# Optimization experiments

Measured on AMD Instinct MI355X. Metric: run time of the kernel, lower is better.

Reference implementation:

```python
import jax, jax.numpy as jnp
import numpy as np

B, S, H, E, I = 2, 2048, 1024, 8, 4096
NUM_SELECT = 2


def setup_inputs() -> dict:
    key = jax.random.key(0)
    ks = jax.random.split(key, 6)
    scale = 0.02
    x = jax.random.normal(ks[0], (B, S, H), dtype=jnp.float32)
    Wg = jax.random.normal(ks[1], (H, E), dtype=jnp.float32) * scale
    W1 = jax.random.normal(ks[2], (E, H, I), dtype=jnp.float32) * scale
    b1 = jnp.zeros((E, I), dtype=jnp.float32)
    W2 = jax.random.normal(ks[3], (E, I, H), dtype=jnp.float32) * scale
    b2 = jnp.zeros((E, H), dtype=jnp.float32)
    return {"x": x, "Wg": Wg, "W1": W1, "b1": b1, "W2": W2, "b2": b2}


def reference(x, Wg, W1, b1, W2, b2):
    b, s, h = x.shape
    e = Wg.shape[1]
    xf = x.reshape(-1, h)                       # [T, H], T = b*s
    T = xf.shape[0]

    logits = xf @ Wg                            # [T, E]
    probs = jax.nn.softmax(logits, axis=-1)
    topk_p, topk_i = jax.lax.top_k(probs, NUM_SELECT)   # [T, k]
    topk_p = topk_p / topk_p.sum(axis=-1, keepdims=True)

    # combine weight per (token, expert): w[t, e] = sum_k topk_p[t, k] * 1[topk_i[t, k] == e]
    # top_k indices within a row are distinct, so scatter-add is exact.
    w = jnp.zeros((T, e), dtype=xf.dtype).at[jnp.arange(T)[:, None], topk_i].add(topk_p)

    # Dense per-expert FFN, weighted combine (weight is 0 for unrouted tokens,
    # so math matches the masked gather/scatter loop of the original).
    out = jnp.zeros_like(xf)
    for ei in range(e):  # small fixed loop over experts
        hdn = jax.nn.silu(xf @ W1[ei] + b1[ei])          # [T, I]
        y = hdn @ W2[ei] + b2[ei]                        # [T, H]
        out = out + w[:, ei:ei + 1] * y
    return out.reshape(b, s, h)
```

## Files before the change

kernel.cpp:

```cpp
#include <hip/hip_runtime.h>
#include <cstdint>
#include <cstddef>

using u16 = unsigned short;
typedef __bf16 bf16x8 __attribute__((ext_vector_type(8)));
typedef float f32x4 __attribute__((ext_vector_type(4)));

#define T_TOK 4096
#define HDIM 1024
#define EXP 8
#define IDIM 4096
#define NROWS 8192
#define PAD_ROWS 8448
#define BM 256
#define MAX_TILES 40

__device__ __forceinline__ u16 f2bf(float f) {
  union { float f; uint32_t u; } v; v.f = f;
  uint32_t u = v.u;
  u += 0x7fffu + ((u >> 16) & 1u);
  return (u16)(u >> 16);
}

__device__ __forceinline__ void async_copy16(const u16* g, u16* s) {
  __builtin_amdgcn_global_load_lds((__attribute__((address_space(1))) void*)(void*)g,
                                   (__attribute__((address_space(3))) void*)s, 16, 0, 0);
}

__global__ __launch_bounds__(256) void gate_kernel(const float* __restrict__ x,
                                                   const float* __restrict__ Wg,
                                                   int* __restrict__ sel_e,
                                                   float* __restrict__ sel_w) {
  int lane = threadIdx.x & 63;
  int wave = threadIdx.x >> 6;
  int t = blockIdx.x * 4 + wave;
  const float* xr = x + (size_t)t * HDIM;
  float p[8];
#pragma unroll
  for (int e = 0; e < 8; ++e) p[e] = 0.f;
#pragma unroll
  for (int i = 0; i < 16; ++i) {
    int h = i * 64 + lane;
    float xv = xr[h];
    const float4* w4 = (const float4*)(Wg + h * 8);
    float4 a = w4[0], b = w4[1];
    p[0] += xv * a.x; p[1] += xv * a.y; p[2] += xv * a.z; p[3] += xv * a.w;
    p[4] += xv * b.x; p[5] += xv * b.y; p[6] += xv * b.z; p[7] += xv * b.w;
  }
#pragma unroll
  for (int e = 0; e < 8; ++e) {
#pragma unroll
    for (int off = 32; off > 0; off >>= 1) p[e] += __shfl_xor(p[e], off);
  }
  if (lane == 0) {
    int e0 = 0; float m0 = p[0];
#pragma unroll
    for (int e = 1; e < 8; ++e) { if (p[e] > m0) { m0 = p[e]; e0 = e; } }
    int e1 = -1; float m1 = -3.4e38f;
#pragma unroll
    for (int e = 0; e < 8; ++e) { if (e != e0 && p[e] > m1) { m1 = p[e]; e1 = e; } }
    float r = expf(m1 - m0);
    float w0 = 1.f / (1.f + r);
    float w1 = r / (1.f + r);
    sel_e[2 * t] = e0; sel_e[2 * t + 1] = e1;
    sel_w[2 * t] = w0; sel_w[2 * t + 1] = w1;
  }
}

__global__ void route_kernel(const int* __restrict__ sel_e, const float* __restrict__ sel_w,
                             int* __restrict__ row_token, float* __restrict__ row_weight,
                             int* __restrict__ tile_e, int* __restrict__ tile_m0,
                             int* __restrict__ tile_nrows, int* __restrict__ num_tiles,
                             int* __restrict__ work_ctr) {
  __shared__ int cnt[EXP], off[EXP], cur[EXP];
  int tid = threadIdx.x;
  if (tid < EXP) { cnt[tid] = 0; cur[tid] = 0; }
  if (tid < 2) work_ctr[tid] = 0;
  __syncthreads();
  for (int i = tid; i < NROWS; i += 256) atomicAdd(&cnt[sel_e[i]], 1);
  __syncthreads();
  if (tid == 0) {
    int running = 0, nt = 0;
    for (int e = 0; e < EXP; ++e) {
      off[e] = running;
      int c = cnt[e];
      int ntile = (c + BM - 1) / BM;
      for (int j = 0; j < ntile; ++j) {
        tile_e[nt] = e;
        tile_m0[nt] = running + j * BM;
        tile_nrows[nt] = min(BM, c - j * BM);
        ++nt;
      }
      running += c;
    }
    *num_tiles = nt;
  }
  __syncthreads();
  for (int i = tid; i < NROWS; i += 256) {
    int e = sel_e[i];
    int pos = off[e] + atomicAdd(&cur[e], 1);
    row_token[pos] = i >> 1;
    row_weight[pos] = sel_w[i];
  }
}

__global__ __launch_bounds__(256) void gather_kernel(const float* __restrict__ x,
                                                     const int* __restrict__ row_token,
                                                     u16* __restrict__ xg) {
  int r = blockIdx.x;
  int tok = row_token[r];
  const float4* xs = (const float4*)(x + (size_t)tok * HDIM);
  float4 v = xs[threadIdx.x];
  ushort4 o;
  o.x = f2bf(v.x); o.y = f2bf(v.y); o.z = f2bf(v.z); o.w = f2bf(v.w);
  *(ushort4*)(xg + (size_t)r * HDIM + threadIdx.x * 4) = o;
}

__global__ __launch_bounds__(256) void transpose_convert(const float* __restrict__ src,
                                                         u16* __restrict__ dst, int R, int C) {
  int eb = blockIdx.z;
  const float* s = src + (size_t)eb * R * C;
  u16* d = dst + (size_t)eb * R * C;
  int cb = blockIdx.x * 64, rb = blockIdx.y * 64;
  __shared__ u16 tile[64][65];
  int tid = threadIdx.x;
#pragma unroll
  for (int i = 0; i < 4; ++i) {
    int idx = i * 256 + tid;
    int r = idx >> 4;
    int cq = (idx & 15) * 4;
    float4 v = *(const float4*)(s + (size_t)(rb + r) * C + cb + cq);
    tile[r][cq]     = f2bf(v.x);
    tile[r][cq + 1] = f2bf(v.y);
    tile[r][cq + 2] = f2bf(v.z);
    tile[r][cq + 3] = f2bf(v.w);
  }
  __syncthreads();
#pragma unroll
  for (int i = 0; i < 4; ++i) {
    int idx = i * 256 + tid;
    int c = idx >> 4;
    int rq = (idx & 15) * 4;
    ushort4 o;
    o.x = tile[rq][c]; o.y = tile[rq + 1][c]; o.z = tile[rq + 2][c]; o.w = tile[rq + 3][c];
    *(ushort4*)(d + (size_t)(cb + c) * R + rb + rq) = o;
  }
}

template <int K, int KS, int NB, bool SECOND>
__global__ __launch_bounds__(512, 2) void ffn_gemm8(
    const u16* __restrict__ A, const u16* __restrict__ B,
    const float* __restrict__ bias, u16* __restrict__ hdn_out,
    float* __restrict__ out, const int* __restrict__ row_token,
    const float* __restrict__ row_weight, const int* __restrict__ tile_e,
    const int* __restrict__ tile_m0, const int* __restrict__ tile_nrows,
    const int* __restrict__ num_tiles, int* __restrict__ work_ctr, int N) {
  constexpr int KT = K / KS / 64;
  constexpr int PER_TILE = NB * KS;

  __shared__ u16 sA[2][2 * 128 * 64];
  __shared__ u16 sB[2][128 * 64];
  __shared__ int s_item;

  int tid = threadIdx.x;
  int lane = tid & 63;
  int wave = tid >> 6;
  int wm = wave >> 2, wn = wave & 3;
  int l15 = lane & 15, quad = lane >> 4;
  int r7 = l15 & 7;

  int c0 = tid, c1 = tid + 512;
  int r0s = c0 >> 3, j0 = ((c0 & 7) ^ (r0s & 7)) * 8;
  int r1s = c1 >> 3, j1 = ((c1 & 7) ^ (r1s & 7)) * 8;

  int jxk[2];
#pragma unroll
  for (int ks = 0; ks < 2; ++ks) jxk[ks] = ((ks * 4 + quad) ^ r7) * 8;

  int total = (*num_tiles) * PER_TILE;

  for (;;) {
    if (tid == 0) s_item = atomicAdd(work_ctr, 1);
    __syncthreads();
    int its = s_item;
    if (its >= total) break;

    int tile = its / PER_TILE;
    int rem = its - tile * PER_TILE;
    int nb = rem % NB;
    int ksp = rem / NB;

    int e = tile_e[tile];
    int row0 = tile_m0[tile];
    int nrows = tile_nrows[tile];
    int n0 = nb * 128;
    int korg = ksp * (K / KS);

    const u16* Ab = A + (size_t)row0 * K + korg;
    const u16* Bb = B + (size_t)e * (size_t)N * K + (size_t)n0 * K + korg;

    auto stageA = [&](int db, int sk, int ha) {
      async_copy16(Ab + (size_t)(ha * 128 + r0s) * K + sk * 64 + j0,
                   &sA[db][ha * 8192 + c0 * 8]);
      async_copy16(Ab + (size_t)(ha * 128 + r1s) * K + sk * 64 + j1,
                   &sA[db][ha * 8192 + c1 * 8]);
    };
    auto stageB = [&](int db, int sk) {
      async_copy16(Bb + (size_t)r0s * K + sk * 64 + j0, &sB[db][c0 * 8]);
      async_copy16(Bb + (size_t)r1s * K + sk * 64 + j1, &sB[db][c1 * 8]);
    };

    f32x4 acc[8][2];
#pragma unroll
    for (int am = 0; am < 8; ++am)
#pragma unroll
      for (int an = 0; an < 2; ++an) acc[am][an] = (f32x4){0.f, 0.f, 0.f, 0.f};

    stageA(0, 0, 0); stageA(0, 0, 1);
    stageB(0, 0);
    stageB(1, 1);
    asm volatile("s_waitcnt vmcnt(2)" ::: "memory");
    __builtin_amdgcn_s_barrier();

    for (int kt = 0; kt < KT; ++kt) {
      int cb = kt & 1, pb = cb ^ 1;
      int ka = kt + 1 < KT ? kt + 1 : KT - 1;
      int kb = kt + 2 < KT ? kt + 2 : KT - 1;
      const u16* sAc = sA[cb];
      const u16* sBc = sB[cb];

      bf16x8 bfr[2][2];
#pragma unroll
      for (int ks = 0; ks < 2; ++ks)
#pragma unroll
        for (int an = 0; an < 2; ++an)
          bfr[an][ks] = *(const bf16x8*)(sBc + ((wn * 2 + an) * 16 + l15) * 64 + jxk[ks]);

      {
        bf16x8 af[4][2];
#pragma unroll
        for (int ks = 0; ks < 2; ++ks)
#pragma unroll
          for (int i = 0; i < 4; ++i)
            af[i][ks] = *(const bf16x8*)(sAc + (wm * 128 + i * 16 + l15) * 64 + jxk[ks]);
        stageA(pb, ka, 0);
        stageA(pb, ka, 1);
        __builtin_amdgcn_s_barrier();
        __builtin_amdgcn_s_setprio(1);
#pragma unroll
        for (int i = 0; i < 4; ++i)
#pragma unroll
          for (int an = 0; an < 2; ++an)
#pragma unroll
            for (int ks = 0; ks < 2; ++ks)
              acc[i][an] = __builtin_amdgcn_mfma_f32_16x16x32_bf16(af[i][ks], bfr[an][ks],
                                                                  acc[i][an], 0, 0, 0);
        __builtin_amdgcn_s_setprio(0);
        __builtin_amdgcn_s_barrier();
      }
      {
        bf16x8 af[4][2];
#pragma unroll
        for (int ks = 0; ks < 2; ++ks)
#pragma unroll
          for (int i = 0; i < 4; ++i)
            af[i][ks] = *(const bf16x8*)(sAc + (wm * 128 + (4 + i) * 16 + l15) * 64 + jxk[ks]);
        stageB(cb, kb);
        asm volatile("s_waitcnt vmcnt(2)" ::: "memory");
        __builtin_amdgcn_s_barrier();
        __builtin_amdgcn_s_setprio(1);
#pragma unroll
        for (int i = 0; i < 4; ++i)
#pragma unroll
          for (int an = 0; an < 2; ++an)
#pragma unroll
            for (int ks = 0; ks < 2; ++ks)
              acc[4 + i][an] = __builtin_amdgcn_mfma_f32_16x16x32_bf16(af[i][ks], bfr[an][ks],
                                                                      acc[4 + i][an], 0, 0, 0);
        __builtin_amdgcn_s_setprio(0);
        __builtin_amdgcn_s_barrier();
      }
    }
    asm volatile("s_waitcnt vmcnt(0)" ::: "memory");

    if constexpr (!SECOND) {
#pragma unroll
      for (int an = 0; an < 2; ++an) {
        int col = n0 + (wn * 2 + an) * 16 + l15;
        float bv = bias[e * N + col];
#pragma unroll
        for (int am = 0; am < 8; ++am) {
#pragma unroll
          for (int r = 0; r < 4; ++r) {
            int lr = wm * 128 + am * 16 + quad * 4 + r;
            if (lr < nrows) {
              float vv = acc[am][an][r] + bv;
              vv = vv / (1.f + __expf(-vv));
              hdn_out[(size_t)(row0 + lr) * N + col] = f2bf(vv);
            }
          }
        }
      }
    } else {
      float bv[2];
#pragma unroll
      for (int an = 0; an < 2; ++an)
        bv[an] = (ksp == 0) ? bias[e * N + n0 + (wn * 2 + an) * 16 + l15] : 0.f;
#pragma unroll
      for (int am = 0; am < 8; ++am) {
#pragma unroll
        for (int r = 0; r < 4; ++r) {
          int lr = wm * 128 + am * 16 + quad * 4 + r;
          if (lr < nrows) {
            int grow = row0 + lr;
            int tok = row_token[grow];
            float w = row_weight[grow];
            float* orow = out + (size_t)tok * N;
#pragma unroll
            for (int an = 0; an < 2; ++an) {
              int col = n0 + (wn * 2 + an) * 16 + l15;
              atomicAdd(orow + col, (acc[am][an][r] + bv[an]) * w);
            }
          }
        }
      }
    }
  }
}

extern "C" void kernel_launch(void* const* d_in, const int* in_sizes, int n_in,
                              void* d_out, int out_size, void* d_ws, size_t ws_size,
                              hipStream_t stream) {
  const float* x  = (const float*)d_in[0];
  const float* Wg = (const float*)d_in[1];
  const float* W1 = (const float*)d_in[2];
  const float* b1 = (const float*)d_in[3];
  const float* W2 = (const float*)d_in[4];
  const float* b2 = (const float*)d_in[5];
  float* out = (float*)d_out;

  char* ws = (char*)d_ws;
  size_t off = 0;
  auto alloc = [&](size_t bytes) {
    void* p = ws + off;
    off += (bytes + 255) & ~(size_t)255;
    return p;
  };
  u16* W1T = (u16*)alloc((size_t)EXP * IDIM * HDIM * 2);
  u16* W2T = (u16*)alloc((size_t)EXP * IDIM * HDIM * 2);
  u16* xg  = (u16*)alloc((size_t)PAD_ROWS * HDIM * 2);
  u16* hdn = (u16*)alloc((size_t)PAD_ROWS * IDIM * 2);
  int*   sel_e      = (int*)alloc(NROWS * 4);
  float* sel_w      = (float*)alloc(NROWS * 4);
  int*   row_token  = (int*)alloc(NROWS * 4);
  float* row_weight = (float*)alloc(NROWS * 4);
  int* tile_e     = (int*)alloc(MAX_TILES * 4);
  int* tile_m0    = (int*)alloc(MAX_TILES * 4);
  int* tile_nrows = (int*)alloc(MAX_TILES * 4);
  int* num_tiles  = (int*)alloc(4);
  int* work_ctr   = (int*)alloc(2 * 4);

  hipMemsetAsync(d_out, 0, (size_t)out_size * sizeof(float), stream);
  transpose_convert<<<dim3(IDIM / 64, HDIM / 64, EXP), 256, 0, stream>>>(W1, W1T, HDIM, IDIM);
  transpose_convert<<<dim3(HDIM / 64, IDIM / 64, EXP), 256, 0, stream>>>(W2, W2T, IDIM, HDIM);
  gate_kernel<<<T_TOK / 4, 256, 0, stream>>>(x, Wg, sel_e, sel_w);
  route_kernel<<<1, 256, 0, stream>>>(sel_e, sel_w, row_token, row_weight,
                                      tile_e, tile_m0, tile_nrows, num_tiles, work_ctr);
  gather_kernel<<<NROWS, 256, 0, stream>>>(x, row_token, xg);
  ffn_gemm8<HDIM, 1, 32, false><<<256, 512, 0, stream>>>(
      xg, W1T, b1, hdn, nullptr, nullptr, nullptr,
      tile_e, tile_m0, tile_nrows, num_tiles, work_ctr + 0, IDIM);
  ffn_gemm8<IDIM, 2, 8, true><<<256, 512, 0, stream>>>(
      hdn, W2T, b2, nullptr, out, row_token, row_weight,
      tile_e, tile_m0, tile_nrows, num_tiles, work_ctr + 1, HDIM);
}
```

Measured before the change: 674.4 us.

## Schedule grouped GEMM work per expert with XCD-affine per-expert work counters

Replaces the single global work counter with eight per-expert counters. Each block starts on the expert matching its XCD index (blockIdx & 7) and moves to the next expert once that one's queue is empty. Within an expert, work items are reordered so the tile index varies fastest, meaning consecutive items share the same weight column block. The aim is to keep each expert's weights resident in one XCD's L2 and to improve weight reuse across tiles. In exchange, blocks may take items from several expert queues near the end, and load balancing is coarser when experts have uneven token counts.

Measured after the change: 682.5 us. About the same (+1.2%).

```diff
diff --git a/kernel.cpp b/kernel.cpp
--- a/kernel.cpp
+++ b/kernel.cpp
@@ -69,13 +69,13 @@
 
 __global__ void route_kernel(const int* __restrict__ sel_e, const float* __restrict__ sel_w,
                              int* __restrict__ row_token, float* __restrict__ row_weight,
-                             int* __restrict__ tile_e, int* __restrict__ tile_m0,
-                             int* __restrict__ tile_nrows, int* __restrict__ num_tiles,
+                             int* __restrict__ tile_m0, int* __restrict__ tile_nrows,
+                             int* __restrict__ tile_start, int* __restrict__ tile_cnt,
                              int* __restrict__ work_ctr) {
   __shared__ int cnt[EXP], off[EXP], cur[EXP];
   int tid = threadIdx.x;
   if (tid < EXP) { cnt[tid] = 0; cur[tid] = 0; }
-  if (tid < 2) work_ctr[tid] = 0;
+  if (tid < 16) work_ctr[tid] = 0;
   __syncthreads();
   for (int i = tid; i < NROWS; i += 256) atomicAdd(&cnt[sel_e[i]], 1);
   __syncthreads();
@@ -85,15 +85,15 @@
       off[e] = running;
       int c = cnt[e];
       int ntile = (c + BM - 1) / BM;
+      tile_start[e] = nt;
+      tile_cnt[e] = ntile;
       for (int j = 0; j < ntile; ++j) {
-        tile_e[nt] = e;
         tile_m0[nt] = running + j * BM;
         tile_nrows[nt] = min(BM, c - j * BM);
         ++nt;
       }
       running += c;
     }
-    *num_tiles = nt;
   }
   __syncthreads();
   for (int i = tid; i < NROWS; i += 256) {
@@ -152,11 +152,10 @@
     const u16* __restrict__ A, const u16* __restrict__ B,
     const float* __restrict__ bias, u16* __restrict__ hdn_out,
     float* __restrict__ out, const int* __restrict__ row_token,
-    const float* __restrict__ row_weight, const int* __restrict__ tile_e,
-    const int* __restrict__ tile_m0, const int* __restrict__ tile_nrows,
-    const int* __restrict__ num_tiles, int* __restrict__ work_ctr, int N) {
+    const float* __restrict__ row_weight, const int* __restrict__ tile_m0,
+    const int* __restrict__ tile_nrows, const int* __restrict__ tile_start,
+    const int* __restrict__ tile_cnt, int* __restrict__ ctr, int N) {
   constexpr int KT = K / KS / 64;
-  constexpr int PER_TILE = NB * KS;
 
   __shared__ u16 sA[2][2 * 128 * 64];
   __shared__ u16 sB[2][128 * 64];
@@ -168,6 +167,7 @@
   int wm = wave >> 2, wn = wave & 3;
   int l15 = lane & 15, quad = lane >> 4;
   int r7 = l15 & 7;
+  int xcd = blockIdx.x & 7;
 
   int c0 = tid, c1 = tid + 512;
   int r0s = c0 >> 3, j0 = ((c0 & 7) ^ (r0s & 7)) * 8;
@@ -177,149 +177,155 @@
 #pragma unroll
   for (int ks = 0; ks < 2; ++ks) jxk[ks] = ((ks * 4 + quad) ^ r7) * 8;
 
-  int total = (*num_tiles) * PER_TILE;
-
-  for (;;) {
-    if (tid == 0) s_item = atomicAdd(work_ctr, 1);
-    __syncthreads();
-    int its = s_item;
-    if (its >= total) break;
-
-    int tile = its / PER_TILE;
-    int rem = its - tile * PER_TILE;
-    int nb = rem % NB;
-    int ksp = rem / NB;
-
-    int e = tile_e[tile];
-    int row0 = tile_m0[tile];
-    int nrows = tile_nrows[tile];
-    int n0 = nb * 128;
-    int korg = ksp * (K / KS);
-
-    const u16* Ab = A + (size_t)row0 * K + korg;
-    const u16* Bb = B + (size_t)e * (size_t)N * K + (size_t)n0 * K + korg;
-
-    auto stageA = [&](int db, int sk, int ha) {
-      async_copy16(Ab + (size_t)(ha * 128 + r0s) * K + sk * 64 + j0,
-                   &sA[db][ha * 8192 + c0 * 8]);
-      async_copy16(Ab + (size_t)(ha * 128 + r1s) * K + sk * 64 + j1,
-                   &sA[db][ha * 8192 + c1 * 8]);
-    };
-    auto stageB = [&](int db, int sk) {
-      async_copy16(Bb + (size_t)r0s * K + sk * 64 + j0, &sB[db][c0 * 8]);
-      async_copy16(Bb + (size_t)r1s * K + sk * 64 + j1, &sB[db][c1 * 8]);
-    };
-
-    f32x4 acc[8][2];
-#pragma unroll
-    for (int am = 0; am < 8; ++am)
-#pragma unroll
-      for (int an = 0; an < 2; ++an) acc[am][an] = (f32x4){0.f, 0.f, 0.f, 0.f};
-
-    stageA(0, 0, 0); stageA(0, 0, 1);
-    stageB(0, 0);
-    stageB(1, 1);
-    asm volatile("s_waitcnt vmcnt(2)" ::: "memory");
-    __builtin_amdgcn_s_barrier();
-
-    for (int kt = 0; kt < KT; ++kt) {
-      int cb = kt & 1, pb = cb ^ 1;
-      int ka = kt + 1 < KT ? kt + 1 : KT - 1;
-      int kb = kt + 2 < KT ? kt + 2 : KT - 1;
-      const u16* sAc = sA[cb];
-      const u16* sBc = sB[cb];
-
-      bf16x8 bfr[2][2];
-#pragma unroll
-      for (int ks = 0; ks < 2; ++ks)
+  for (int pass = 0; pass < 8; ++pass) {
+    int ex = (xcd + pass) & 7;
+    int nt_e = tile_cnt[ex];
+    if (nt_e == 0) continue;
+    int items = nt_e * NB * KS;
+    int ts = tile_start[ex];
+
+    for (;;) {
+      if (tid == 0) s_item = atomicAdd(&ctr[ex], 1);
+      __syncthreads();
+      int its = s_item;
+      if (its >= items) break;
+
+      int per = NB * nt_e;
+      int ksp = its / per;
+      int rem = its - ksp * per;
+      int nb = rem / nt_e;
+      int tile = ts + (rem - nb * nt_e);
+
+      int row0 = tile_m0[tile];
+      int nrows = tile_nrows[tile];
+      int n0 = nb * 128;
+      int korg = ksp * (K / KS);
+
+      const u16* Ab = A + (size_t)row0 * K + korg;
+      const u16* Bb = B + (size_t)ex * (size_t)N * K + (size_t)n0 * K + korg;
+
+      auto stageA = [&](int db, int sk, int ha) {
+        async_copy16(Ab + (size_t)(ha * 128 + r0s) * K + sk * 64 + j0,
+                     &sA[db][ha * 8192 + c0 * 8]);
+        async_copy16(Ab + (size_t)(ha * 128 + r1s) * K + sk * 64 + j1,
+                     &sA[db][ha * 8192 + c1 * 8]);
+      };
+      auto stageB = [&](int db, int sk) {
+        async_copy16(Bb + (size_t)r0s * K + sk * 64 + j0, &sB[db][c0 * 8]);
+        async_copy16(Bb + (size_t)r1s * K + sk * 64 + j1, &sB[db][c1 * 8]);
+      };
+
+      f32x4 acc[8][2];
+#pragma unroll
+      for (int am = 0; am < 8; ++am)
+#pragma unroll
+        for (int an = 0; an < 2; ++an) acc[am][an] = (f32x4){0.f, 0.f, 0.f, 0.f};
+
+      stageA(0, 0, 0); stageA(0, 0, 1);
+      stageB(0, 0);
+      stageB(1, 1);
+      asm volatile("s_waitcnt vmcnt(2)" ::: "memory");
+      __builtin_amdgcn_s_barrier();
+
+      for (int kt = 0; kt < KT; ++kt) {
+        int cb = kt & 1, pb = cb ^ 1;
+        int ka = kt + 1 < KT ? kt + 1 : KT - 1;
+        int kb = kt + 2 < KT ? kt + 2 : KT - 1;
+        const u16* sAc = sA[cb];
+        const u16* sBc = sB[cb];
+
+        bf16x8 bfr[2][2];
+#pragma unroll
+        for (int ks = 0; ks < 2; ++ks)
+#pragma unroll
+          for (int an = 0; an < 2; ++an)
+            bfr[an][ks] = *(const bf16x8*)(sBc + ((wn * 2 + an) * 16 + l15) * 64 + jxk[ks]);
+
+        {
+          bf16x8 af[4][2];
+#pragma unroll
+          for (int ks = 0; ks < 2; ++ks)
+#pragma unroll
+            for (int i = 0; i < 4; ++i)
+              af[i][ks] = *(const bf16x8*)(sAc + (wm * 128 + i * 16 + l15) * 64 + jxk[ks]);
+          stageA(pb, ka, 0);
+          stageA(pb, ka, 1);
+          __builtin_amdgcn_s_barrier();
+          __builtin_amdgcn_s_setprio(1);
+#pragma unroll
+          for (int i = 0; i < 4; ++i)
+#pragma unroll
+            for (int an = 0; an < 2; ++an)
+#pragma unroll
+              for (int ks = 0; ks < 2; ++ks)
+                acc[i][an] = __builtin_amdgcn_mfma_f32_16x16x32_bf16(af[i][ks], bfr[an][ks],
+                                                                    acc[i][an], 0, 0, 0);
+          __builtin_amdgcn_s_setprio(0);
+          __builtin_amdgcn_s_barrier();
+        }
+        {
+          bf16x8 af[4][2];
+#pragma unroll
+          for (int ks = 0; ks < 2; ++ks)
+#pragma unroll
+            for (int i = 0; i < 4; ++i)
+              af[i][ks] = *(const bf16x8*)(sAc + (wm * 128 + (4 + i) * 16 + l15) * 64 + jxk[ks]);
+          stageB(cb, kb);
+          asm volatile("s_waitcnt vmcnt(2)" ::: "memory");
+          __builtin_amdgcn_s_barrier();
+          __builtin_amdgcn_s_setprio(1);
+#pragma unroll
+          for (int i = 0; i < 4; ++i)
+#pragma unroll
+            for (int an = 0; an < 2; ++an)
+#pragma unroll
+              for (int ks = 0; ks < 2; ++ks)
+                acc[4 + i][an] = __builtin_amdgcn_mfma_f32_16x16x32_bf16(af[i][ks], bfr[an][ks],
+                                                                        acc[4 + i][an], 0, 0, 0);
+          __builtin_amdgcn_s_setprio(0);
+          __builtin_amdgcn_s_barrier();
+        }
+      }
+      asm volatile("s_waitcnt vmcnt(0)" ::: "memory");
+
+      if constexpr (!SECOND) {
+#pragma unroll
+        for (int an = 0; an < 2; ++an) {
+          int col = n0 + (wn * 2 + an) * 16 + l15;
+          float bv = bias[ex * N + col];
+#pragma unroll
+          for (int am = 0; am < 8; ++am) {
+#pragma unroll
+            for (int r = 0; r < 4; ++r) {
+              int lr = wm * 128 + am * 16 + quad * 4 + r;
+              if (lr < nrows) {
+                float vv = acc[am][an][r] + bv;
+                vv = vv / (1.f + __expf(-vv));
+                hdn_out[(size_t)(row0 + lr) * N + col] = f2bf(vv);
+              }
+            }
+          }
+        }
+      } else {
+        float bv[2];
 #pragma unroll
         for (int an = 0; an < 2; ++an)
-          bfr[an][ks] = *(const bf16x8*)(sBc + ((wn * 2 + an) * 16 + l15) * 64 + jxk[ks]);
-
-      {
-        bf16x8 af[4][2];
-#pragma unroll
-        for (int ks = 0; ks < 2; ++ks)
-#pragma unroll
-          for (int i = 0; i < 4; ++i)
-            af[i][ks] = *(const bf16x8*)(sAc + (wm * 128 + i * 16 + l15) * 64 + jxk[ks]);
-        stageA(pb, ka, 0);
-        stageA(pb, ka, 1);
-        __builtin_amdgcn_s_barrier();
-        __builtin_amdgcn_s_setprio(1);
-#pragma unroll
-        for (int i = 0; i < 4; ++i)
-#pragma unroll
-          for (int an = 0; an < 2; ++an)
-#pragma unroll
-            for (int ks = 0; ks < 2; ++ks)
-              acc[i][an] = __builtin_amdgcn_mfma_f32_16x16x32_bf16(af[i][ks], bfr[an][ks],
-                                                                  acc[i][an], 0, 0, 0);
-        __builtin_amdgcn_s_setprio(0);
-        __builtin_amdgcn_s_barrier();
-      }
-      {
-        bf16x8 af[4][2];
-#pragma unroll
-        for (int ks = 0; ks < 2; ++ks)
-#pragma unroll
-          for (int i = 0; i < 4; ++i)
-            af[i][ks] = *(const bf16x8*)(sAc + (wm * 128 + (4 + i) * 16 + l15) * 64 + jxk[ks]);
-        stageB(cb, kb);
-        asm volatile("s_waitcnt vmcnt(2)" ::: "memory");
-        __builtin_amdgcn_s_barrier();
-        __builtin_amdgcn_s_setprio(1);
-#pragma unroll
-        for (int i = 0; i < 4; ++i)
-#pragma unroll
-          for (int an = 0; an < 2; ++an)
-#pragma unroll
-            for (int ks = 0; ks < 2; ++ks)
-              acc[4 + i][an] = __builtin_amdgcn_mfma_f32_16x16x32_bf16(af[i][ks], bfr[an][ks],
-                                                                      acc[4 + i][an], 0, 0, 0);
-        __builtin_amdgcn_s_setprio(0);
-        __builtin_amdgcn_s_barrier();
-      }
-    }
-    asm volatile("s_waitcnt vmcnt(0)" ::: "memory");
-
-    if constexpr (!SECOND) {
-#pragma unroll
-      for (int an = 0; an < 2; ++an) {
-        int col = n0 + (wn * 2 + an) * 16 + l15;
-        float bv = bias[e * N + col];
+          bv[an] = (ksp == 0) ? bias[ex * N + n0 + (wn * 2 + an) * 16 + l15] : 0.f;
 #pragma unroll
         for (int am = 0; am < 8; ++am) {
 #pragma unroll
           for (int r = 0; r < 4; ++r) {
             int lr = wm * 128 + am * 16 + quad * 4 + r;
             if (lr < nrows) {
-              float vv = acc[am][an][r] + bv;
-              vv = vv / (1.f + __expf(-vv));
-              hdn_out[(size_t)(row0 + lr) * N + col] = f2bf(vv);
-            }
-          }
-        }
-      }
-    } else {
-      float bv[2];
-#pragma unroll
-      for (int an = 0; an < 2; ++an)
-        bv[an] = (ksp == 0) ? bias[e * N + n0 + (wn * 2 + an) * 16 + l15] : 0.f;
-#pragma unroll
-      for (int am = 0; am < 8; ++am) {
-#pragma unroll
-        for (int r = 0; r < 4; ++r) {
-          int lr = wm * 128 + am * 16 + quad * 4 + r;
-          if (lr < nrows) {
-            int grow = row0 + lr;
-            int tok = row_token[grow];
-            float w = row_weight[grow];
-            float* orow = out + (size_t)tok * N;
-#pragma unroll
-            for (int an = 0; an < 2; ++an) {
-              int col = n0 + (wn * 2 + an) * 16 + l15;
-              atomicAdd(orow + col, (acc[am][an][r] + bv[an]) * w);
+              int grow = row0 + lr;
+              int tok = row_token[grow];
+              float w = row_weight[grow];
+              float* orow = out + (size_t)tok * N;
+#pragma unroll
+              for (int an = 0; an < 2; ++an) {
+                int col = n0 + (wn * 2 + an) * 16 + l15;
+                atomicAdd(orow + col, (acc[am][an][r] + bv[an]) * w);
+              }
             }
           }
         }
@@ -354,23 +360,23 @@
   float* sel_w      = (float*)alloc(NROWS * 4);
   int*   row_token  = (int*)alloc(NROWS * 4);
   float* row_weight = (float*)alloc(NROWS * 4);
-  int* tile_e     = (int*)alloc(MAX_TILES * 4);
   int* tile_m0    = (int*)alloc(MAX_TILES * 4);
   int* tile_nrows = (int*)alloc(MAX_TILES * 4);
-  int* num_tiles  = (int*)alloc(4);
-  int* work_ctr   = (int*)alloc(2 * 4);
+  int* tile_start = (int*)alloc(EXP * 4);
+  int* tile_cnt   = (int*)alloc(EXP * 4);
+  int* work_ctr   = (int*)alloc(16 * 4);
 
   hipMemsetAsync(d_out, 0, (size_t)out_size * sizeof(float), stream);
   transpose_convert<<<dim3(IDIM / 64, HDIM / 64, EXP), 256, 0, stream>>>(W1, W1T, HDIM, IDIM);
   transpose_convert<<<dim3(HDIM / 64, IDIM / 64, EXP), 256, 0, stream>>>(W2, W2T, IDIM, HDIM);
   gate_kernel<<<T_TOK / 4, 256, 0, stream>>>(x, Wg, sel_e, sel_w);
   route_kernel<<<1, 256, 0, stream>>>(sel_e, sel_w, row_token, row_weight,
-                                      tile_e, tile_m0, tile_nrows, num_tiles, work_ctr);
+                                      tile_m0, tile_nrows, tile_start, tile_cnt, work_ctr);
   gather_kernel<<<NROWS, 256, 0, stream>>>(x, row_token, xg);
   ffn_gemm8<HDIM, 1, 32, false><<<256, 512, 0, stream>>>(
       xg, W1T, b1, hdn, nullptr, nullptr, nullptr,
-      tile_e, tile_m0, tile_nrows, num_tiles, work_ctr + 0, IDIM);
+      tile_m0, tile_nrows, tile_start, tile_cnt, work_ctr + 0, IDIM);
   ffn_gemm8<IDIM, 2, 8, true><<<256, 512, 0, stream>>>(
       hdn, W2T, b2, nullptr, out, row_token, row_weight,
-      tile_e, tile_m0, tile_nrows, num_tiles, work_ctr + 1, HDIM);
-}
+      tile_m0, tile_nrows, tile_start, tile_cnt, work_ctr + 8, HDIM);
+}
```
